# Performance work log

Hardware: AMD Instinct MI355X
Metric: run time of the kernel (lower is better)

The kernel has to match this reference:

```python
import jax, jax.numpy as jnp
import numpy as np

DIM = 1024
HEADS = 16
HEAD_DIM = DIM // HEADS


def setup_inputs() -> dict:
    key = jax.random.key(0)
    ks = jax.random.split(key, 9)
    s = 1.0 / np.sqrt(DIM)
    return {
        "x": jax.random.normal(ks[0], (2, 2048, 1, DIM), dtype=jnp.float32),
        "Wq": jax.random.normal(ks[1], (DIM, DIM), dtype=jnp.float32) * s,
        "bq": jnp.zeros((DIM,), dtype=jnp.float32),
        "Wk": jax.random.normal(ks[2], (DIM, DIM), dtype=jnp.float32) * s,
        "bk": jnp.zeros((DIM,), dtype=jnp.float32),
        "Wv": jax.random.normal(ks[3], (DIM, DIM), dtype=jnp.float32) * s,
        "bv": jnp.zeros((DIM,), dtype=jnp.float32),
        "Wo": jax.random.normal(ks[4], (DIM, DIM), dtype=jnp.float32) * s,
        "bo": jnp.zeros((DIM,), dtype=jnp.float32),
    }


def reference(x, Wq, bq, Wk, bk, Wv, bv, Wo, bo):
    b, t, _, d = x.shape
    h, hd = HEADS, HEAD_DIM
    # torch Linear: y = x @ W.T + b
    q = (x @ Wq.T + bq).reshape(b, t, h, hd)
    k = (x @ Wk.T + bk).reshape(b, t, h, hd)
    v = (x @ Wv.T + bv).reshape(b, t, h, hd)
    # Source applies self.scaling (hd**-0.5) in torch AND divides by
    # sqrt(k_features) inside the jax chunk routine -> net scale 1/hd.
    q = q * (1.0 / hd)
    # key_chunk_size >= T -> one chunk; online softmax == exact stable softmax
    scores = jnp.einsum('bqhd,bkhd->bhqk', q, k)  # [B,H,T,T]
    w = jax.nn.softmax(scores, axis=-1)
    o = jnp.einsum('bhqk,bkhd->bqhd', w, v).reshape(b, t, d)
    return o @ Wo.T + bo
```

## Files before the change

### kernel.cpp

```cpp
#include <hip/hip_runtime.h>
#include <math.h>

typedef _Float16 f16;
typedef _Float16 f16x2 __attribute__((ext_vector_type(2)));
typedef _Float16 f16x4 __attribute__((ext_vector_type(4)));
typedef _Float16 f16x8 __attribute__((ext_vector_type(8)));
typedef float    f32x4 __attribute__((ext_vector_type(4)));

constexpr int DIM   = 1024;
constexpr int HEADS = 16;
constexpr int HD    = 64;
constexpr int BATCH = 2;
constexpr int SEQ   = 2048;
constexpr int MTOT  = BATCH * SEQ;
constexpr int NT    = SEQ / 64;

#define QSCALE (1.4426950408889634f / 64.0f)

#define MFMA16(a, b, c) __builtin_amdgcn_mfma_f32_16x16x32_f16((a), (b), (c), 0, 0, 0)
#define SPLIT2(x, hh, ll) { const float _t = (x); hh = (f16)_t; ll = (f16)(_t - (float)(hh)); }

__device__ __forceinline__ void glds16(const void* g, void* l) {
    __builtin_amdgcn_global_load_lds(
        (const __attribute__((address_space(1))) void*)g,
        (__attribute__((address_space(3))) void*)l, 16, 0, 0);
}

__device__ __forceinline__ float exp2_hw(float x) {
    float r;
    asm("v_exp_f32 %0, %1" : "=v"(r) : "v"(x));
    return r;
}

__device__ __forceinline__ f16x2 pk_f16(float a, float b) {
    return __builtin_bit_cast(f16x2, __builtin_amdgcn_cvt_pkrtz(a, b));
}

__global__ __launch_bounds__(256) void presplit_kernel(
    const float* __restrict__ x,  const float* __restrict__ Wq,
    const float* __restrict__ Wk, const float* __restrict__ Wv,
    const float* __restrict__ Wo,
    f16* __restrict__ Xh,  f16* __restrict__ WqH, f16* __restrict__ WkH,
    f16* __restrict__ WvH, f16* __restrict__ WoH, f16* __restrict__ WoL)
{
    const int bid = blockIdx.x;
    const float* src; f16* dh; f16* dl = nullptr; int row;
    if (bid < 4096)      { src = x;  dh = Xh;  row = bid; }
    else if (bid < 5120) { src = Wq; dh = WqH; row = bid - 4096; }
    else if (bid < 6144) { src = Wk; dh = WkH; row = bid - 5120; }
    else if (bid < 7168) { src = Wv; dh = WvH; row = bid - 6144; }
    else                 { src = Wo; dh = WoH; dl = WoL; row = bid - 7168; }

    const int k = threadIdx.x * 4;
    const float4 v = *reinterpret_cast<const float4*>(&src[(size_t)row * DIM + k]);
    const int s = (row >> 1) & 3;
    const size_t o = (size_t)row * DIM + (k & ~31) + ((k & 31) ^ (s << 3));
    if (dl) {
        f16x4 h4, l4;
        SPLIT2(v.x, h4[0], l4[0]); SPLIT2(v.y, h4[1], l4[1]);
        SPLIT2(v.z, h4[2], l4[2]); SPLIT2(v.w, h4[3], l4[3]);
        *reinterpret_cast<f16x4*>(&dh[o]) = h4;
        *reinterpret_cast<f16x4*>(&dl[o]) = l4;
    } else {
        f16x4 h4;
        h4[0] = (f16)v.x; h4[1] = (f16)v.y; h4[2] = (f16)v.z; h4[3] = (f16)v.w;
        *reinterpret_cast<f16x4*>(&dh[o]) = h4;
    }
}

template <int MODE, int TERMS>
__device__ __forceinline__ void gemm_plane_body(
    const f16* __restrict__ AhG, const f16* __restrict__ BhG,
    const f16* __restrict__ BlG, const float* __restrict__ bias,
    float* __restrict__ C, f16* __restrict__ F, float scale,
    f16* __restrict__ smem)
{
    f16* Ah = smem;
    f16* Bh = smem + 4096;
    f16* Bl = smem + 8192;

    const int tid = threadIdx.x;
    const int l   = tid & 63;
    const int w   = tid >> 6;
    const int wm  = (w >> 1) * 64;
    const int wn  = (w & 1) * 64;
    const int m0  = blockIdx.y * 128;
    const int n0  = blockIdx.x * 128;
    const int fr  = l & 15;
    const int fk  = (l >> 4) * 8;
    const int rg  = (l >> 4) * 4;
    const int fko = fk ^ (((fr >> 1) & 3) << 3);

    f32x4 acc[4][4] = {};

    for (int k0 = 0; k0 < DIM; k0 += 32) {
        __syncthreads();
        constexpr int NCH = (TERMS == 1) ? 4 : 6;
        #pragma unroll
        for (int j = 0; j < NCH; ++j) {
            const int c = w * NCH + j;
            const int p = c >> 3;
            const f16* P = (p == 0) ? AhG : (p == 1) ? BhG : BlG;
            const int r0 = (p == 0) ? m0 : n0;
            const int row = r0 + (c & 7) * 16 + (l >> 2);
            glds16(P + (size_t)row * DIM + k0 + (l & 3) * 8, smem + c * 512);
        }
        asm volatile("s_waitcnt vmcnt(0)" ::: "memory");
        __syncthreads();

        f16x8 ah[4], bh[4], bl[4];
        #pragma unroll
        for (int m = 0; m < 4; ++m)
            ah[m] = *reinterpret_cast<const f16x8*>(&Ah[(wm + m * 16 + fr) * 32 + fko]);
        #pragma unroll
        for (int n = 0; n < 4; ++n) {
            const int r = (wn + n * 16 + fr) * 32 + fko;
            bh[n] = *reinterpret_cast<const f16x8*>(&Bh[r]);
            if (TERMS == 2) bl[n] = *reinterpret_cast<const f16x8*>(&Bl[r]);
        }
        #pragma unroll
        for (int n = 0; n < 4; ++n) {
            #pragma unroll
            for (int m = 0; m < 4; ++m) {
                if (MODE == 1) {
                    acc[m][n] = MFMA16(bh[n], ah[m], acc[m][n]);
                } else {
                    acc[m][n] = MFMA16(ah[m], bh[n], acc[m][n]);
                    if (TERMS == 2)
                        acc[m][n] = MFMA16(ah[m], bl[n], acc[m][n]);
                }
            }
        }
    }

    if (MODE == 0 || MODE == 3) {
        #pragma unroll
        for (int n = 0; n < 4; ++n) {
            const int col  = n0 + wn + n * 16 + fr;
            const float bb = bias[col];
            #pragma unroll
            for (int m = 0; m < 4; ++m) {
                #pragma unroll
                for (int r = 0; r < 4; ++r) {
                    const int row = m0 + wm + m * 16 + rg + r;
                    const float v = (acc[m][n][r] + bb) * scale;
                    if (MODE == 0) C[(size_t)row * DIM + col] = v;
                    else           F[(size_t)row * DIM + col] = (f16)v;
                }
            }
        }
    } else if (MODE == 1) {
        constexpr int RS = 72;
        const int batch = m0 >> 11;
        const int kvg0  = m0 & 2047;
        for (int s = 0; s < 2; ++s) {
            __syncthreads();
            if ((w & 1) == s) {
                #pragma unroll
                for (int n = 0; n < 4; ++n) {
                    #pragma unroll
                    for (int m = 0; m < 4; ++m) {
                        const int kvrow = wm + m * 16 + fr;
                        const int dd    = n * 16 + rg;
                        f16x4 h4;
                        #pragma unroll
                        for (int r = 0; r < 4; ++r)
                            h4[r] = (f16)(acc[m][n][r] + bias[n0 + wn + dd + r]);
                        const int o = kvrow * RS + (dd ^ ((kvrow & 7) << 3));
                        *reinterpret_cast<f16x4*>(&smem[o]) = h4;
                    }
                }
            }
            __syncthreads();
            const size_t bh_ = (size_t)batch * HEADS + (n0 >> 6) + s;
            const int row = tid >> 1, c0 = (tid & 1) * 32;
            #pragma unroll
            for (int j = 0; j < 4; ++j) {
                const int so = row * RS + c0 + j * 8;
                const size_t go = bh_ * 131072 + (size_t)(kvg0 + row) * 64 + c0 + j * 8;
                *reinterpret_cast<f16x8*>(&F[go]) =
                    *reinterpret_cast<const f16x8*>(&smem[so]);
            }
        }
    } else {
        constexpr int RS = 136;
        const int batch = m0 >> 11;
        const int kvg0  = m0 & 2047;
        for (int s = 0; s < 2; ++s) {
            __syncthreads();
            if ((w & 1) == s) {
                #pragma unroll
                for (int n = 0; n < 4; ++n) {
                    const int d    = n * 16 + fr;
                    const float bb = bias[n0 + wn + d];
                    #pragma unroll
                    for (int m = 0; m < 4; ++m) {
                        const int kvl = wm + m * 16 + rg;
                        f16x4 h4;
                        h4[0] = (f16)(acc[m][n][0] + bb);
                        h4[1] = (f16)(acc[m][n][1] + bb);
                        h4[2] = (f16)(acc[m][n][2] + bb);
                        h4[3] = (f16)(acc[m][n][3] + bb);
                        const int o = d * RS + (kvl ^ ((d & 7) << 3));
                        *reinterpret_cast<f16x4*>(&smem[o]) = h4;
                    }
                }
            }
            __syncthreads();
            const size_t bh_ = (size_t)batch * HEADS + (n0 >> 6) + s;
            const int row = tid >> 2, c0 = (tid & 3) * 32;
            #pragma unroll
            for (int j = 0; j < 4; ++j) {
                const int so = row * RS + c0 + j * 8;
                const size_t go = bh_ * 131072 + (size_t)row * 2048 + kvg0 + c0 + j * 8;
                *reinterpret_cast<f16x8*>(&F[go]) =
                    *reinterpret_cast<const f16x8*>(&smem[so]);
            }
        }
    }
}

__global__ __launch_bounds__(256) void qkv_kernel(
    const f16* __restrict__ XhG,
    const f16* __restrict__ WqH, const float* __restrict__ bq,
    const f16* __restrict__ WkH, const float* __restrict__ bk,
    const f16* __restrict__ WvH, const float* __restrict__ bv,
    f16* __restrict__ QhG, f16* __restrict__ KhG, f16* __restrict__ VhG)
{
    __shared__ __align__(16) f16 smem[9216];
    if (blockIdx.z == 0)
        gemm_plane_body<3, 1>(XhG, WqH, nullptr, bq, nullptr, QhG, QSCALE, smem);
    else if (blockIdx.z == 1)
        gemm_plane_body<1, 1>(XhG, WkH, nullptr, bk, nullptr, KhG, 1.0f, smem);
    else
        gemm_plane_body<2, 1>(XhG, WvH, nullptr, bv, nullptr, VhG, 1.0f, smem);
}

__global__ __launch_bounds__(256) void oproj_kernel(
    const f16* __restrict__ OhG,
    const f16* __restrict__ WoH, const f16* __restrict__ WoL,
    const float* __restrict__ bo, float* __restrict__ out)
{
    __shared__ __align__(16) f16 smem[12288];
    gemm_plane_body<0, 2>(OhG, WoH, WoL, bo, out, nullptr, 1.0f, smem);
}

__global__ __launch_bounds__(256, 4) void attn_kernel(
    const f16* __restrict__ QhG, const f16* __restrict__ KhG,
    const f16* __restrict__ VhG, f16* __restrict__ OhG)
{
    __shared__ __align__(16) f16 lds[2][2][4096];
    __shared__ __align__(16) f16 PL[4][1024];

    const int tid = threadIdx.x;
    const int l   = tid & 63;
    const int w   = tid >> 6;
    const int fr  = l & 15;
    const int g   = l >> 4;
    const int fk  = g * 8;
    const int rg  = g * 4;
    const int swz = (fr & 7) << 3;

    const int lin  = blockIdx.x + 32 * (blockIdx.y + 16 * blockIdx.z);
    const int sid  = (lin & 7) * 128 + (lin >> 3);
    const int qblk = sid & 31;
    const int head = (sid >> 5) & 15;
    const int batch = sid >> 9;

    const int q0 = qblk * 64;
    const size_t rowbase = (size_t)batch * SEQ;
    const int hcol = head * HD;
    const size_t bhbase = ((size_t)batch * HEADS + head) * (size_t)(SEQ * HD);

    size_t kA[2], vA[2];
    #pragma unroll
    for (int c = 0; c < 2; ++c) {
        const int h0 = (w * 2 + c) * 512 + l * 8;
        kA[c] = bhbase + (size_t)h0;
        vA[c] = bhbase + (size_t)(h0 >> 6) * 2048 + (h0 & 63);
    }

#define STAGE(B, T) do {                                                    \
        const size_t _ko = (size_t)(T) * 4096;                              \
        const size_t _vo = (size_t)(T) * 64;                                \
        _Pragma("unroll")                                                   \
        for (int c = 0; c < 2; ++c) {                                       \
            const int lo_ = (w * 2 + c) * 512;                              \
            glds16(KhG + kA[c] + _ko, &lds[B][0][lo_]);                     \
            glds16(VhG + vA[c] + _vo, &lds[B][1][lo_]);                     \
        }                                                                   \
    } while (0)

    STAGE(0, 0);

    f16x8 qh[2];
    {
        const f16* qp = &QhG[(rowbase + q0 + w * 16 + fr) * DIM + hcol];
        qh[0] = *reinterpret_cast<const f16x8*>(&qp[fk]);
        qh[1] = *reinterpret_cast<const f16x8*>(&qp[32 + fk]);
    }

    f16x8 onesv;
    #pragma unroll
    for (int i = 0; i < 8; ++i) onesv[i] = (f16)1.0f;

    f32x4 ls = {};
    f32x4 oa[4] = {};

    int cur = 0;
    for (int t = 0; t < NT; ++t) {
        asm volatile("s_waitcnt vmcnt(0) lgkmcnt(0)\ns_barrier" ::: "memory");
        if (t + 1 < NT) STAGE(cur ^ 1, t + 1);

        const f16* Kh = &lds[cur][0][0];
        const f16* Vh = &lds[cur][1][0];

        f32x4 sa[4] = {};
        __builtin_amdgcn_s_setprio(1);
        #pragma unroll
        for (int kvb = 0; kvb < 4; ++kvb) {
            #pragma unroll
            for (int ks = 0; ks < 2; ++ks) {
                const int o = ((kvb * 16 + fr) * 64 + ks * 32 + fk) ^ swz;
                const f16x8 kh = *reinterpret_cast<const f16x8*>(&Kh[o]);
                sa[kvb] = MFMA16(kh, qh[ks], sa[kvb]);
            }
        }
        __builtin_amdgcn_s_setprio(0);

        f16* Wh = &PL[w][0];
        #pragma unroll
        for (int kvb = 0; kvb < 4; ++kvb) {
            const f16x2 p01 = pk_f16(exp2_hw(sa[kvb][0]), exp2_hw(sa[kvb][1]));
            const f16x2 p23 = pk_f16(exp2_hw(sa[kvb][2]), exp2_hw(sa[kvb][3]));
            f16x4 h4;
            h4[0] = p01[0]; h4[1] = p01[1]; h4[2] = p23[0]; h4[3] = p23[1];
            const int po = (fr * 64 + kvb * 16 + rg) ^ swz;
            *reinterpret_cast<f16x4*>(&Wh[po]) = h4;
        }

        f16x8 pf[2];
        #pragma unroll
        for (int ks = 0; ks < 2; ++ks) {
            const int ro = (fr * 64 + ks * 32 + fk) ^ swz;
            pf[ks] = *reinterpret_cast<const f16x8*>(&Wh[ro]);
        }

        __builtin_amdgcn_s_setprio(1);
        #pragma unroll
        for (int ks = 0; ks < 2; ++ks)
            ls = MFMA16(onesv, pf[ks], ls);
        #pragma unroll
        for (int db = 0; db < 4; ++db) {
            #pragma unroll
            for (int ks = 0; ks < 2; ++ks) {
                const int vo = ((db * 16 + fr) * 64 + ks * 32 + fk) ^ swz;
                const f16x8 vh = *reinterpret_cast<const f16x8*>(&Vh[vo]);
                oa[db] = MFMA16(vh, pf[ks], oa[db]);
            }
        }
        __builtin_amdgcn_s_setprio(0);
        cur ^= 1;
    }
#undef STAGE

    const float inv = 1.0f / ls[0];
    const size_t row = rowbase + q0 + w * 16 + fr;
    const int s = ((int)row >> 1) & 3;
    #pragma unroll
    for (int db = 0; db < 4; ++db) {
        f16x4 h4;
        #pragma unroll
        for (int j = 0; j < 4; ++j) h4[j] = (f16)(oa[db][j] * inv);
        const int kg = hcol + db * 16 + rg;
        const size_t o = row * DIM + (kg & ~31) + ((kg & 31) ^ (s << 3));
        *reinterpret_cast<f16x4*>(&OhG[o]) = h4;
    }
}

extern "C" void kernel_launch(void* const* d_in, const int* in_sizes, int n_in,
                              void* d_out, int out_size, void* d_ws, size_t ws_size,
                              hipStream_t stream)
{
    const float* x  = (const float*)d_in[0];
    const float* Wq = (const float*)d_in[1];
    const float* bq = (const float*)d_in[2];
    const float* Wk = (const float*)d_in[3];
    const float* bk = (const float*)d_in[4];
    const float* Wv = (const float*)d_in[5];
    const float* bv = (const float*)d_in[6];
    const float* Wo = (const float*)d_in[7];
    const float* bo = (const float*)d_in[8];
    float* out = (float*)d_out;

    const size_t PS = (size_t)MTOT * DIM;
    f16* QhG = (f16*)d_ws;
    f16* KhG = QhG + PS;
    f16* VhG = KhG + PS;
    f16* XhG = VhG + PS;
    f16* WqH = XhG + PS;
    f16* WkH = WqH + (size_t)DIM * DIM;
    f16* WvH = WkH + (size_t)DIM * DIM;
    f16* WoH = WvH + (size_t)DIM * DIM;
    f16* WoL = WoH + (size_t)DIM * DIM;
    f16* OhG = XhG;

    presplit_kernel<<<8192, 256, 0, stream>>>(x, Wq, Wk, Wv, Wo,
                                              XhG, WqH, WkH, WvH, WoH, WoL);

    dim3 gqkv(DIM / 128, MTOT / 128, 3);
    qkv_kernel<<<gqkv, 256, 0, stream>>>(XhG, WqH, bq, WkH, bk, WvH, bv,
                                         QhG, KhG, VhG);

    dim3 gattn(SEQ / 64, HEADS, BATCH);
    attn_kernel<<<gattn, 256, 0, stream>>>(QhG, KhG, VhG, OhG);

    dim3 gout(DIM / 128, MTOT / 128);
    oproj_kernel<<<gout, 256, 0, stream>>>(OhG, WoH, WoL, bo, out);
}
```

Measured before the change: 135.0 us.

## Process two 16-row query blocks per wave to reuse K/V tiles in attention

Each attention workgroup now handles 128 query rows instead of 64, with every wave computing two 16-row query sub-blocks against the same K and V fragments loaded from LDS. This halves the number of workgroups and the total global K/V staging traffic, and reuses each K/V LDS read for two MFMAs. In exchange it doubles accumulator registers, lowers the occupancy hint to 2 blocks per CU, and leaves 512 blocks, which may underfill the GPU's CUs.

```diff
diff --git a/kernel.cpp b/kernel.cpp
--- a/kernel.cpp
+++ b/kernel.cpp
@@ -245,12 +245,12 @@
     gemm_plane_body<0, 2>(OhG, WoH, WoL, bo, out, nullptr, 1.0f, smem);
 }
 
-__global__ __launch_bounds__(256, 4) void attn_kernel(
+__global__ __launch_bounds__(256, 2) void attn_kernel(
     const f16* __restrict__ QhG, const f16* __restrict__ KhG,
     const f16* __restrict__ VhG, f16* __restrict__ OhG)
 {
     __shared__ __align__(16) f16 lds[2][2][4096];
-    __shared__ __align__(16) f16 PL[4][1024];
+    __shared__ __align__(16) f16 PL[4][2][1024];
 
     const int tid = threadIdx.x;
     const int l   = tid & 63;
@@ -261,13 +261,13 @@
     const int rg  = g * 4;
     const int swz = (fr & 7) << 3;
 
-    const int lin  = blockIdx.x + 32 * (blockIdx.y + 16 * blockIdx.z);
-    const int sid  = (lin & 7) * 128 + (lin >> 3);
-    const int qblk = sid & 31;
-    const int head = (sid >> 5) & 15;
-    const int batch = sid >> 9;
-
-    const int q0 = qblk * 64;
+    const int lin  = blockIdx.x + 16 * (blockIdx.y + 16 * blockIdx.z);
+    const int sid  = (lin & 7) * 64 + (lin >> 3);
+    const int qblk = sid & 15;
+    const int head = (sid >> 4) & 15;
+    const int batch = sid >> 8;
+
+    const int q0 = qblk * 128;
     const size_t rowbase = (size_t)batch * SEQ;
     const int hcol = head * HD;
     const size_t bhbase = ((size_t)batch * HEADS + head) * (size_t)(SEQ * HD);
@@ -293,19 +293,20 @@
 
     STAGE(0, 0);
 
-    f16x8 qh[2];
-    {
-        const f16* qp = &QhG[(rowbase + q0 + w * 16 + fr) * DIM + hcol];
-        qh[0] = *reinterpret_cast<const f16x8*>(&qp[fk]);
-        qh[1] = *reinterpret_cast<const f16x8*>(&qp[32 + fk]);
+    f16x8 qh[2][2];
+    #pragma unroll
+    for (int qb = 0; qb < 2; ++qb) {
+        const f16* qp = &QhG[(rowbase + q0 + w * 32 + qb * 16 + fr) * DIM + hcol];
+        qh[qb][0] = *reinterpret_cast<const f16x8*>(&qp[fk]);
+        qh[qb][1] = *reinterpret_cast<const f16x8*>(&qp[32 + fk]);
     }
 
     f16x8 onesv;
     #pragma unroll
     for (int i = 0; i < 8; ++i) onesv[i] = (f16)1.0f;
 
-    f32x4 ls = {};
-    f32x4 oa[4] = {};
+    f32x4 ls[2] = {};
+    f32x4 oa[4][2] = {};
 
     int cur = 0;
     for (int t = 0; t < NT; ++t) {
@@ -315,7 +316,7 @@
         const f16* Kh = &lds[cur][0][0];
         const f16* Vh = &lds[cur][1][0];
 
-        f32x4 sa[4] = {};
+        f32x4 sa[4][2] = {};
         __builtin_amdgcn_s_setprio(1);
         #pragma unroll
         for (int kvb = 0; kvb < 4; ++kvb) {
@@ -323,40 +324,48 @@
             for (int ks = 0; ks < 2; ++ks) {
                 const int o = ((kvb * 16 + fr) * 64 + ks * 32 + fk) ^ swz;
                 const f16x8 kh = *reinterpret_cast<const f16x8*>(&Kh[o]);
-                sa[kvb] = MFMA16(kh, qh[ks], sa[kvb]);
+                sa[kvb][0] = MFMA16(kh, qh[0][ks], sa[kvb][0]);
+                sa[kvb][1] = MFMA16(kh, qh[1][ks], sa[kvb][1]);
             }
         }
         __builtin_amdgcn_s_setprio(0);
 
-        f16* Wh = &PL[w][0];
-        #pragma unroll
-        for (int kvb = 0; kvb < 4; ++kvb) {
-            const f16x2 p01 = pk_f16(exp2_hw(sa[kvb][0]), exp2_hw(sa[kvb][1]));
-            const f16x2 p23 = pk_f16(exp2_hw(sa[kvb][2]), exp2_hw(sa[kvb][3]));
-            f16x4 h4;
-            h4[0] = p01[0]; h4[1] = p01[1]; h4[2] = p23[0]; h4[3] = p23[1];
-            const int po = (fr * 64 + kvb * 16 + rg) ^ swz;
-            *reinterpret_cast<f16x4*>(&Wh[po]) = h4;
-        }
-
-        f16x8 pf[2];
-        #pragma unroll
-        for (int ks = 0; ks < 2; ++ks) {
-            const int ro = (fr * 64 + ks * 32 + fk) ^ swz;
-            pf[ks] = *reinterpret_cast<const f16x8*>(&Wh[ro]);
+        f16x8 pf[2][2];
+        #pragma unroll
+        for (int qb = 0; qb < 2; ++qb) {
+            f16* Wh = &PL[w][qb][0];
+            #pragma unroll
+            for (int kvb = 0; kvb < 4; ++kvb) {
+                const f16x2 p01 = pk_f16(exp2_hw(sa[kvb][qb][0]),
+                                         exp2_hw(sa[kvb][qb][1]));
+                const f16x2 p23 = pk_f16(exp2_hw(sa[kvb][qb][2]),
+                                         exp2_hw(sa[kvb][qb][3]));
+                f16x4 h4;
+                h4[0] = p01[0]; h4[1] = p01[1]; h4[2] = p23[0]; h4[3] = p23[1];
+                const int po = (fr * 64 + kvb * 16 + rg) ^ swz;
+                *reinterpret_cast<f16x4*>(&Wh[po]) = h4;
+            }
+            #pragma unroll
+            for (int ks = 0; ks < 2; ++ks) {
+                const int ro = (fr * 64 + ks * 32 + fk) ^ swz;
+                pf[qb][ks] = *reinterpret_cast<const f16x8*>(&Wh[ro]);
+            }
         }
 
         __builtin_amdgcn_s_setprio(1);
         #pragma unroll
-        for (int ks = 0; ks < 2; ++ks)
-            ls = MFMA16(onesv, pf[ks], ls);
+        for (int qb = 0; qb < 2; ++qb)
+            #pragma unroll
+            for (int ks = 0; ks < 2; ++ks)
+                ls[qb] = MFMA16(onesv, pf[qb][ks], ls[qb]);
         #pragma unroll
         for (int db = 0; db < 4; ++db) {
             #pragma unroll
             for (int ks = 0; ks < 2; ++ks) {
                 const int vo = ((db * 16 + fr) * 64 + ks * 32 + fk) ^ swz;
                 const f16x8 vh = *reinterpret_cast<const f16x8*>(&Vh[vo]);
-                oa[db] = MFMA16(vh, pf[ks], oa[db]);
+                oa[db][0] = MFMA16(vh, pf[0][ks], oa[db][0]);
+                oa[db][1] = MFMA16(vh, pf[1][ks], oa[db][1]);
             }
         }
         __builtin_amdgcn_s_setprio(0);
@@ -364,17 +373,20 @@
     }
 #undef STAGE
 
-    const float inv = 1.0f / ls[0];
-    const size_t row = rowbase + q0 + w * 16 + fr;
-    const int s = ((int)row >> 1) & 3;
     #pragma unroll
-    for (int db = 0; db < 4; ++db) {
-        f16x4 h4;
-        #pragma unroll
-        for (int j = 0; j < 4; ++j) h4[j] = (f16)(oa[db][j] * inv);
-        const int kg = hcol + db * 16 + rg;
-        const size_t o = row * DIM + (kg & ~31) + ((kg & 31) ^ (s << 3));
-        *reinterpret_cast<f16x4*>(&OhG[o]) = h4;
+    for (int qb = 0; qb < 2; ++qb) {
+        const float inv = 1.0f / ls[qb][0];
+        const size_t row = rowbase + q0 + w * 32 + qb * 16 + fr;
+        const int s = ((int)row >> 1) & 3;
+        #pragma unroll
+        for (int db = 0; db < 4; ++db) {
+            f16x4 h4;
+            #pragma unroll
+            for (int j = 0; j < 4; ++j) h4[j] = (f16)(oa[db][qb][j] * inv);
+            const int kg = hcol + db * 16 + rg;
+            const size_t o = row * DIM + (kg & ~31) + ((kg & 31) ^ (s << 3));
+            *reinterpret_cast<f16x4*>(&OhG[o]) = h4;
+        }
     }
 }
 
@@ -412,7 +424,7 @@
     qkv_kernel<<<gqkv, 256, 0, stream>>>(XhG, WqH, bq, WkH, bk, WvH, bv,
                                          QhG, KhG, VhG);
 
-    dim3 gattn(SEQ / 64, HEADS, BATCH);
+    dim3 gattn(SEQ / 128, HEADS, BATCH);
     attn_kernel<<<gattn, 256, 0, stream>>>(QhG, KhG, VhG, OhG);
 
     dim3 gout(DIM / 128, MTOT / 128);
```

Measured after the change: 127.9 us. 1.06x faster.
